# Performance work log

Hardware: AMD Instinct MI355X
Metric: run time of the kernel (lower is better)

## Reference

```python
import jax, jax.numpy as jnp
import numpy as np

B, N, IN, E, H, F = 64, 256, 128, 256, 8, 1024


def setup_inputs() -> dict:
    key = jax.random.key(0)
    ks = jax.random.split(key, 16)
    x = jax.random.normal(ks[0], (B, N, IN), jnp.float32)
    adj = (jax.random.uniform(ks[1], (B, N, N)) < 0.1).astype(jnp.float32)
    adj = jnp.maximum(adj, adj.transpose(0, 2, 1))  # symmetric 0/1 adjacency
    mask = jax.random.randint(ks[2], (B, N), 0, 2).astype(jnp.float32)
    dist = jax.random.normal(ks[3], (B, N, N), jnp.float32)

    def lin(k, i, o):
        return (jax.random.normal(k, (i, o), jnp.float32) / np.sqrt(i)).astype(jnp.float32)

    return dict(
        x=x, adj=adj, mask=mask, dist=dist,
        W1=lin(ks[4], IN, E), b1=jnp.zeros((E,), jnp.float32),
        W2=lin(ks[5], E, E), b2=jnp.zeros((E,), jnp.float32),
        W3=lin(ks[6], E, E), b3=jnp.zeros((E,), jnp.float32),
        ln1_g=jnp.ones((E,), jnp.float32), ln1_b=jnp.zeros((E,), jnp.float32),
        Wq=lin(ks[7], E, H * E), Wk=lin(ks[8], E, H * E), Wv=lin(ks[9], E, H * E),
        Wo=lin(ks[10], H * E, E), bo=jnp.zeros((E,), jnp.float32),
        ln2_g=jnp.ones((E,), jnp.float32), ln2_b=jnp.zeros((E,), jnp.float32),
        Wf1=lin(ks[11], E, F), bf1=jnp.zeros((F,), jnp.float32),
        Wf2=lin(ks[12], F, E), bf2=jnp.zeros((E,), jnp.float32),
    )


def _layernorm(x, g, b):
    m = x.mean(-1, keepdims=True)
    v = ((x - m) ** 2).mean(-1, keepdims=True)
    return (x - m) * jax.lax.rsqrt(v + 1e-5) * g + b


def reference(x, adj, mask, dist, W1, b1, W2, b2, W3, b3, ln1_g, ln1_b,
              Wq, Wk, Wv, Wo, bo, ln2_g, ln2_b, Wf1, bf1, Wf2, bf2):
    # --- DenseGCNConv normalization (add self-loops, sym-normalize) ---
    eye = jnp.eye(N, dtype=adj.dtype)
    A = adj * (1.0 - eye) + eye                      # fill_diag(adj, 1)
    dis = jax.lax.rsqrt(jnp.clip(A.sum(-1), 1.0, None))
    An = dis[:, :, None] * A * dis[:, None, :]       # D^-1/2 A D^-1/2, [B,N,N]
    m3 = mask[:, :, None]

    def gcn(h, W, b):
        return (jnp.einsum('bij,bjf->bif', An, h @ W) + b) * m3

    g1 = jax.nn.relu(gcn(x, W1, b1))
    g2 = jax.nn.relu(gcn(g1, W2, b2))
    g3 = jax.nn.relu(gcn(g2, W3, b3))
    gcn_res = g1 + g2 + g3

    # --- masked MHA with distance bias (head dim = E per head) ---
    h = _layernorm(gcn_res, ln1_g, ln1_b)
    mh = mask[:, None, :, None]                      # [B,1,N,1]
    q = (h @ Wq).reshape(B, N, H, E).transpose(0, 2, 1, 3) * mh
    k = (h @ Wk).reshape(B, N, H, E).transpose(0, 2, 1, 3) * mh
    v = (h @ Wv).reshape(B, N, H, E).transpose(0, 2, 1, 3) * mh
    a = jnp.einsum('bhne,bhme->bhnm', q * (E ** -0.5), k) + dist[:, None]
    am = (mask[:, :, None] * mask[:, None, :])[:, None]  # [B,1,N,N]
    a = jnp.where(am == 0, -1e9, a)
    a = jax.nn.softmax(a, axis=-1)
    a = jnp.where(am == 0, 0.0, a)
    y = jnp.einsum('bhnm,bhme->bhne', a, v).transpose(0, 2, 1, 3).reshape(B, N, H * E)
    y = (y @ Wo + bo) * m3
    att = gcn_res + y

    # --- FFN block ---
    f = _layernorm(att, ln2_g, ln2_b)
    f = (jax.nn.gelu(f @ Wf1 + bf1, approximate=False) @ Wf2 + bf2) * m3
    att = att + f
    return gcn_res + att
```

## Files before the change

### kernel.cpp

```cpp
#include <hip/hip_runtime.h>
#include <hip/hip_bf16.h>
#include <cmath>

#define BB 64
#define NNODES 256
#define INF_ 128
#define EE 256
#define HH 8
#define FFN 1024
#define BNROWS 16384

typedef __attribute__((ext_vector_type(8))) short short8;
typedef __attribute__((ext_vector_type(4))) float floatx4;
typedef __attribute__((ext_vector_type(4))) unsigned short ushort4v;

__device__ __forceinline__ float b2f(unsigned short u) {
  union { unsigned u32; float f; } w; w.u32 = ((unsigned)u) << 16; return w.f;
}
__device__ __forceinline__ unsigned short f2b(float f) {
  union { float f; unsigned u32; } w; w.f = f;
  unsigned r = w.u32 + 0x7FFFu + ((w.u32 >> 16) & 1u);
  return (unsigned short)(r >> 16);
}
__device__ __forceinline__ float gelu_f(float x) {
  const float z = 0.7978845608028654f * (x + 0.044715f * x * x * x);
  const float e = __expf(2.0f * z);
  const float th = (e - 1.0f) / (e + 1.0f);
  return 0.5f * x * (1.0f + th);
}

typedef const __attribute__((address_space(1))) void GV;
typedef __attribute__((address_space(3))) void LV;

__device__ __forceinline__ void gl_lds16(const unsigned short* g,
                                         unsigned short* l, int lane) {
#if __has_builtin(__builtin_amdgcn_global_load_lds)
  __builtin_amdgcn_global_load_lds((GV*)g, (LV*)l, 16, 0, 0);
#else
  *(short8*)(l + lane * 8) = *(const short8*)g;
#endif
}

#define VMW2() asm volatile("s_waitcnt vmcnt(2)" ::: "memory")
#define VMW0() asm volatile("s_waitcnt vmcnt(0)" ::: "memory")
#define LGW0() asm volatile("s_waitcnt lgkmcnt(0)" ::: "memory")
#define MBAR() do { asm volatile("" ::: "memory"); \
                    __builtin_amdgcn_s_barrier(); \
                    asm volatile("" ::: "memory"); } while (0)

struct PackArgs {
  const float* src[12];
  unsigned short* dst[12];
  int R[12], C[12];
  int start[13];
};

__launch_bounds__(256)
__global__ void pack_kernel(PackArgs a)
{
  __shared__ float tile[32][33];
  const int bid = blockIdx.x;
  int j = 0;
  while (bid >= a.start[j + 1]) j++;
  const int lb = bid - a.start[j];
  const float* src = a.src[j];
  unsigned short* dst = a.dst[j];
  const int R = a.R[j], C = a.C[j];

  if (C == 0) {
    const int i = (lb * 256 + threadIdx.x) * 4;
    if (i >= R) return;
    floatx4 v = *(const floatx4*)(src + i);
    ushort4v o;
    #pragma unroll
    for (int k = 0; k < 4; k++) o[k] = f2b(v[k]);
    *(ushort4v*)(dst + i) = o;
    return;
  }
  const int tpr = C >> 5;
  const int c0 = (lb % tpr) * 32, r0 = (lb / tpr) * 32;
  const int tx = threadIdx.x & 31, ty = threadIdx.x >> 5;
  #pragma unroll
  for (int i = ty; i < 32; i += 8)
    tile[i][tx] = src[(long long)(r0 + i) * C + c0 + tx];
  __syncthreads();
  #pragma unroll
  for (int i = ty; i < 32; i += 8)
    dst[(long long)(c0 + i) * R + r0 + tx] = f2b(tile[tx][i]);
}

__global__ void deg_kernel(const float* __restrict__ adj,
                           float* __restrict__ dis)
{
  const int g = blockIdx.x * 4 + (threadIdx.x >> 6);
  const int lane = threadIdx.x & 63;
  const int i = g & 255;
  floatx4 v = *(const floatx4*)(adj + (long long)g * 256 + lane * 4);
  float s = 0.f;
  #pragma unroll
  for (int jj = 0; jj < 4; jj++) {
    const int j = lane * 4 + jj;
    s += (j == i) ? 1.0f : v[jj];
  }
  #pragma unroll
  for (int off = 32; off > 0; off >>= 1) s += __shfl_xor(s, off);
  if (lane == 0) dis[g] = 1.0f / sqrtf(fmaxf(s, 1.0f));
}

__global__ void an_kernel(const float* __restrict__ adj,
                          const float* __restrict__ dis,
                          unsigned short* __restrict__ An)
{
  const long long base = ((long long)blockIdx.x * 256 + threadIdx.x) * 4;
  const int rowg = (int)(base >> 8);
  const int i = rowg & 255;
  const int brow = rowg & ~255;
  const int j0 = (int)(base & 255);
  const float di = dis[rowg];
  floatx4 v = *(const floatx4*)(adj + base);
  ushort4v o;
  #pragma unroll
  for (int jj = 0; jj < 4; jj++) {
    const int j = j0 + jj;
    const float a = (j == i) ? 1.0f : v[jj];
    o[jj] = f2b(di * dis[brow + j] * a);
  }
  *(ushort4v*)(An + base) = o;
}

__launch_bounds__(512, 4)
__global__ void gemm_kernel(const unsigned short* __restrict__ A, int lda,
                            long long sAo, long long sAi,
                            const unsigned short* __restrict__ Bm, int ldb,
                            long long sBo, long long sBi,
                            void* __restrict__ Cv, int ldc,
                            long long sCo, long long sCi,
                            int K, int zshift, int mode, int flag,
                            const float* __restrict__ aux1,
                            const float* __restrict__ mask,
                            float* __restrict__ gcn,
                            void* __restrict__ aux2)
{
  __shared__ __align__(16) unsigned short sA[16384];
  __shared__ __align__(16) unsigned short sB[16384];

  const int t = threadIdx.x;
  const int z = blockIdx.z;
  const int zi = z & ((1 << zshift) - 1);
  const int zb = z >> zshift;
  const int m0 = blockIdx.x * 128;
  const int n0 = blockIdx.y * 128;
  A  += zb * sAo + zi * sAi;
  Bm += zb * sBo + zi * sBi;
  const long long cbase = zb * sCo + zi * sCi;

  const int lane = t & 63;
  const int w = t >> 6;
  const int wm = w >> 2, wn = w & 3;
  const int lm = lane & 15, qd = lane >> 4;

  floatx4 acc[4][2] = {};

  const int sub = lane >> 4;
  const int qs  = lane & 15;
  const unsigned short* pA[4];
  const unsigned short* pB[4];
  #pragma unroll
  for (int i = 0; i < 4; i++) {
    const int d = w * 4 + i;
    const int r = d * 4 + sub;
    const int co = (qs ^ (r & 7)) * 8;
    pA[i] = A + (long long)(m0 + r) * lda + co;
    pB[i] = Bm + (long long)(n0 + r) * ldb + co;
  }

  for (int kk = 0; kk < K; kk += 128) {
    #pragma unroll
    for (int i = 0; i < 4; i++) {
      gl_lds16(pA[i] + kk, &sA[(w * 4 + i) * 512], lane);
      gl_lds16(pB[i] + kk, &sB[(w * 4 + i) * 512], lane);
    }
    __syncthreads();

    #pragma unroll
    for (int ks = 0; ks < 4; ks++) {
      short8 af[4], bg[2];
      const int q = ks * 4 + qd;
      #pragma unroll
      for (int mi = 0; mi < 4; mi++) {
        const int r = wm * 64 + mi * 16 + lm;
        af[mi] = *(const short8*)&sA[r * 128 + ((q ^ (r & 7)) * 8)];
      }
      #pragma unroll
      for (int ni = 0; ni < 2; ni++) {
        const int r = wn * 32 + ni * 16 + lm;
        bg[ni] = *(const short8*)&sB[r * 128 + ((q ^ (r & 7)) * 8)];
      }
      #pragma unroll
      for (int mi = 0; mi < 4; mi++)
        #pragma unroll
        for (int ni = 0; ni < 2; ni++)
          acc[mi][ni] = __builtin_amdgcn_mfma_f32_16x16x32_bf16(
              af[mi], bg[ni], acc[mi][ni], 0, 0, 0);
    }
    __syncthreads();
  }

  #pragma unroll
  for (int mi = 0; mi < 4; mi++) {
    const int row0 = m0 + wm * 64 + mi * 16 + qd * 4;
    #pragma unroll
    for (int ni = 0; ni < 2; ni++) {
      const int col = n0 + wn * 32 + ni * 16 + lm;
      floatx4 a = acc[mi][ni];
      if (mode == 0) {
        float* Cf = (float*)Cv;
        #pragma unroll
        for (int r = 0; r < 4; r++)
          Cf[cbase + (long long)(row0 + r) * ldc + col] = a[r];
      } else if (mode == 1) {
        unsigned short* Cb = (unsigned short*)Cv;
        #pragma unroll
        for (int r = 0; r < 4; r++)
          Cb[cbase + (long long)(row0 + r) * ldc + col] = f2b(a[r]);
      } else if (mode == 2) {
        float* Cf = (float*)Cv;
        #pragma unroll
        for (int r = 0; r < 4; r++)
          Cf[cbase + (long long)(row0 + r) * ldc + col] += a[r];
      } else if (mode == 3) {
        unsigned short* Cb = (unsigned short*)Cv;
        const float bv = aux1[col];
        #pragma unroll
        for (int r = 0; r < 4; r++)
          Cb[cbase + (long long)(row0 + r) * ldc + col] = f2b(gelu_f(a[r] + bv));
      } else if (mode == 5) {
        const int b = row0 >> 8, n = row0 & 255;
        ushort4v o;
        #pragma unroll
        for (int r = 0; r < 4; r++) o[r] = f2b(a[r]);
        *(ushort4v*)((unsigned short*)Cv + (long long)b * 65536 + col * 256 + n) = o;
      } else if (mode == 8) {
        float* Cf = (float*)Cv;
        const float* attf = (const float*)aux2;
        const float bv = aux1[col];
        #pragma unroll
        for (int r = 0; r < 4; r++) {
          const long long idx = (long long)(row0 + r) * 256 + col;
          Cf[idx] = gcn[idx] + attf[idx] + (a[r] + bv) * mask[row0 + r];
        }
      } else if (mode == 9) {
        const int token = zb * 256 + col;
        const float m = mask[token];
        ushort4v o; floatx4 g;
        #pragma unroll
        for (int r = 0; r < 4; r++) {
          const float v = fmaxf((a[r] + aux1[row0 + r]) * m, 0.f);
          o[r] = f2b(v); g[r] = v;
        }
        *(ushort4v*)((unsigned short*)Cv + (long long)token * 256 + row0) = o;
        float* gp = gcn + (long long)token * 256 + row0;
        if (flag) { floatx4 old = *(const floatx4*)gp; g += old; }
        *(floatx4*)gp = g;
      } else if (mode == 12) {
        float* Cf = (float*)Cv;
        const float bv = aux1[col];
        #pragma unroll
        for (int r = 0; r < 4; r++) {
          const long long idx = (long long)(row0 + r) * 256 + col;
          Cf[idx] = gcn[idx] + (a[r] + bv) * mask[row0 + r];
        }
      } else if (mode == 13) {
        unsigned short* Cb = (unsigned short*)Cv;
        #pragma unroll
        for (int r = 0; r < 4; r++)
          Cb[cbase + (long long)(row0 + r) * ldc + col] = f2b(a[r] * 0.0625f);
      } else {
        const int z2 = (row0 >> 8) * 8 + (col >> 8);
        const int e = col & 255, n = row0 & 255;
        ushort4v o;
        #pragma unroll
        for (int r = 0; r < 4; r++) o[r] = f2b(a[r]);
        *(ushort4v*)((unsigned short*)aux2 + (long long)z2 * 65536 + e * 256 + n) = o;
      }
    }
  }
}

__launch_bounds__(512, 4)
__global__ void attn_kernel(unsigned short* __restrict__ QP,
                            const unsigned short* __restrict__ HBF,
                            const unsigned short* __restrict__ ABH,
                            const unsigned short* __restrict__ VT,
                            const unsigned short* __restrict__ DSTB,
                            const float* __restrict__ mask)
{
  __shared__ __align__(16) unsigned short sR0[16896];
  __shared__ __align__(16) unsigned short sS[16384];
  __shared__ float redm[4][64];
  __shared__ float reds[4][64];

  const int bi = blockIdx.x;
  const int x  = bi & 7;
  const int seq = bi >> 3;
  const int b  = (seq >> 5) * 8 + x;
  const int h  = (seq >> 2) & 7;
  const int mt = seq & 3;
  const int m0 = mt * 64;
  const int z = b * 8 + h;

  const int t = threadIdx.x, lane = t & 63, w = t >> 6;
  const int lm = lane & 15, qd = lane >> 4;
  const int wm2 = w >> 2, wn4 = w & 3;

  unsigned short* Ym = QP + ((long long)(b * 256 + m0)) * 2048 + h * 256;
  const unsigned short* Hb = HBF + (long long)b * 65536;
  const unsigned short* Hq = Hb + (long long)m0 * 256;
  const unsigned short* Ah = ABH + (long long)h * 65536;
  const unsigned short* Vb = VT + (long long)z * 65536;
  const unsigned short* db = DSTB + (long long)b * 65536 + (long long)m0 * 256;
  const float* maskb = mask + b * 256;

  floatx4 S[2][4];
  #pragma unroll
  for (int mi = 0; mi < 2; mi++)
    #pragma unroll
    for (int ni = 0; ni < 4; ni++) {
      const int col = wn4 * 64 + ni * 16 + lm;
      #pragma unroll
      for (int r = 0; r < 4; r++) {
        const int row = wm2 * 32 + mi * 16 + qd * 4 + r;
        S[mi][ni][r] = b2f(db[row * 256 + col]);
      }
    }

  int eoff0, eoff1;
  {
    const int rA = lane >> 2, sl = lane & 3;
    const int r0 = (w * 2 + 0) * 16 + rA;
    const int r1 = (w * 2 + 1) * 16 + rA;
    eoff0 = r0 * 256 + ((sl ^ ((r0 >> 1) & 3)) * 8);
    eoff1 = r1 * 256 + ((sl ^ ((r1 >> 1) & 3)) * 8);
  }
  const int ld0 = (w * 2 + 0) * 512;
  const int ld1 = (w * 2 + 1) * 512;

  auto STAGE = [&](int c) {
    const unsigned short* bp =
        (c < 8 ? Ah : (c < 16 ? Hb : Vb)) + (c & 7) * 32;
    const int bb = (c & 1) * 8192;
    gl_lds16(bp + eoff0, &sS[bb + ld0], lane);
    gl_lds16(bp + eoff1, &sS[bb + ld1], lane);
  };

  {
    const int rin2 = lane >> 5, qs32 = lane & 31;
    #pragma unroll
    for (int i = 0; i < 4; i++) {
      const int d = w * 4 + i;
      const int r = d * 2 + rin2;
      gl_lds16(Hq + (long long)r * 256 + ((qs32 ^ (r & 7)) * 8),
               &sR0[d * 512], lane);
    }
  }
  STAGE(0); STAGE(1);
  VMW2();
  MBAR();

  floatx4 accq[2][4] = {};
  #pragma unroll
  for (int c = 0; c < 8; c++) {
    __builtin_amdgcn_s_setprio(1);
    short8 af[2], bg[4];
    #pragma unroll
    for (int mi = 0; mi < 2; mi++) {
      const int r = wm2 * 32 + mi * 16 + lm;
      const int q = c * 4 + qd;
      af[mi] = *(const short8*)&sR0[r * 256 + ((q ^ (r & 7)) * 8)];
    }
    const int bb = (c & 1) * 8192;
    #pragma unroll
    for (int ni = 0; ni < 4; ni++) {
      const int rr = wn4 * 64 + ni * 16 + lm;
      bg[ni] = *(const short8*)&sS[bb + rr * 32 + ((qd ^ ((rr >> 1) & 3)) * 8)];
    }
    #pragma unroll
    for (int mi = 0; mi < 2; mi++)
      #pragma unroll
      for (int ni = 0; ni < 4; ni++)
        accq[mi][ni] = __builtin_amdgcn_mfma_f32_16x16x32_bf16(
            af[mi], bg[ni], accq[mi][ni], 0, 0, 0);
    __builtin_amdgcn_s_setprio(0);
    MBAR();
    STAGE(c + 2);
    VMW2();
    MBAR();
  }

  #pragma unroll
  for (int mi = 0; mi < 2; mi++)
    #pragma unroll
    for (int rr = 0; rr < 4; rr++) {
      const int row = wm2 * 32 + mi * 16 + qd * 4 + rr;
      #pragma unroll
      for (int ni = 0; ni < 4; ni++) {
        const int col = wn4 * 64 + ni * 16 + lm;
        const int o = col >> 3;
        sR0[row * 256 + ((o ^ (row & 7)) * 8) + (col & 7)] = f2b(accq[mi][ni][rr]);
      }
    }
  LGW0();
  MBAR();

  #pragma unroll
  for (int c = 8; c < 16; c++) {
    __builtin_amdgcn_s_setprio(1);
    short8 af[2], bg[4];
    #pragma unroll
    for (int mi = 0; mi < 2; mi++) {
      const int r = wm2 * 32 + mi * 16 + lm;
      const int q = (c - 8) * 4 + qd;
      af[mi] = *(const short8*)&sR0[r * 256 + ((q ^ (r & 7)) * 8)];
    }
    const int bb = (c & 1) * 8192;
    #pragma unroll
    for (int ni = 0; ni < 4; ni++) {
      const int rr = wn4 * 64 + ni * 16 + lm;
      bg[ni] = *(const short8*)&sS[bb + rr * 32 + ((qd ^ ((rr >> 1) & 3)) * 8)];
    }
    #pragma unroll
    for (int mi = 0; mi < 2; mi++)
      #pragma unroll
      for (int ni = 0; ni < 4; ni++)
        S[mi][ni] = __builtin_amdgcn_mfma_f32_16x16x32_bf16(
            af[mi], bg[ni], S[mi][ni], 0, 0, 0);
    __builtin_amdgcn_s_setprio(0);
    MBAR();
    STAGE(c + 2);
    VMW2();
    MBAR();
  }

  float mkv[4];
  #pragma unroll
  for (int ni = 0; ni < 4; ni++) mkv[ni] = maskb[wn4 * 64 + ni * 16 + lm];

  float lred[2][4];
  #pragma unroll
  for (int mi = 0; mi < 2; mi++) {
    #pragma unroll
    for (int r = 0; r < 4; r++) {
      const int row = wm2 * 32 + mi * 16 + qd * 4 + r;
      const float mq = maskb[m0 + row];
      float mx = -3e38f;
      #pragma unroll
      for (int ni = 0; ni < 4; ni++) {
        const float v = (mq != 0.f && mkv[ni] != 0.f) ? S[mi][ni][r] : -1e9f;
        S[mi][ni][r] = v;
        mx = fmaxf(mx, v);
      }
      lred[mi][r] = mx;
    }
  }
  #pragma unroll
  for (int off = 1; off < 16; off <<= 1)
    #pragma unroll
    for (int mi = 0; mi < 2; mi++)
      #pragma unroll
      for (int r = 0; r < 4; r++)
        lred[mi][r] = fmaxf(lred[mi][r], __shfl_xor(lred[mi][r], off));
  if (lm == 0)
    #pragma unroll
    for (int mi = 0; mi < 2; mi++)
      #pragma unroll
      for (int r = 0; r < 4; r++)
        redm[wn4][wm2 * 32 + mi * 16 + qd * 4 + r] = lred[mi][r];
  LGW0();
  MBAR();

  #pragma unroll
  for (int mi = 0; mi < 2; mi++) {
    #pragma unroll
    for (int r = 0; r < 4; r++) {
      const int row = wm2 * 32 + mi * 16 + qd * 4 + r;
      const float gmax = fmaxf(fmaxf(redm[0][row], redm[1][row]),
                               fmaxf(redm[2][row], redm[3][row]));
      float ss = 0.f;
      #pragma unroll
      for (int ni = 0; ni < 4; ni++) {
        const float e = __expf(S[mi][ni][r] - gmax);
        S[mi][ni][r] = e;
        ss += e;
      }
      lred[mi][r] = ss;
    }
  }
  #pragma unroll
  for (int off = 1; off < 16; off <<= 1)
    #pragma unroll
    for (int mi = 0; mi < 2; mi++)
      #pragma unroll
      for (int r = 0; r < 4; r++)
        lred[mi][r] += __shfl_xor(lred[mi][r], off);
  if (lm == 0)
    #pragma unroll
    for (int mi = 0; mi < 2; mi++)
      #pragma unroll
      for (int r = 0; r < 4; r++)
        reds[wn4][wm2 * 32 + mi * 16 + qd * 4 + r] = lred[mi][r];
  LGW0();
  MBAR();

  #pragma unroll
  for (int mi = 0; mi < 2; mi++)
    #pragma unroll
    for (int r = 0; r < 4; r++) {
      const int row = wm2 * 32 + mi * 16 + qd * 4 + r;
      const float inv = 1.0f / (reds[0][row] + reds[1][row] +
                                reds[2][row] + reds[3][row]);
      #pragma unroll
      for (int ni = 0; ni < 4; ni++) {
        const int kl = ni * 16 + lm;
        const int slot = (kl >> 3) ^ (row & 7);
        sR0[wn4 * 4096 + row * 64 + slot * 8 + (kl & 7)] =
            f2b(S[mi][ni][r] * inv);
      }
    }
  LGW0();
  MBAR();

  floatx4 Y[2][4] = {};
  #pragma unroll
  for (int c = 16; c < 24; c++) {
    __builtin_amdgcn_s_setprio(1);
    const int pp = (c - 16) >> 1;
    const int op = ((c - 16) & 1) * 4 + qd;
    short8 af[2], bg[4];
    #pragma unroll
    for (int mi = 0; mi < 2; mi++) {
      const int r = wm2 * 32 + mi * 16 + lm;
      af[mi] = *(const short8*)&sR0[pp * 4096 + r * 64 + ((op ^ (r & 7)) * 8)];
    }
    const int bb = (c & 1) * 8192;
    #pragma unroll
    for (int ni = 0; ni < 4; ni++) {
      const int rr = wn4 * 64 + ni * 16 + lm;
      bg[ni] = *(const short8*)&sS[bb + rr * 32 + ((qd ^ ((rr >> 1) & 3)) * 8)];
    }
    #pragma unroll
    for (int mi = 0; mi < 2; mi++)
      #pragma unroll
      for (int ni = 0; ni < 4; ni++)
        Y[mi][ni] = __builtin_amdgcn_mfma_f32_16x16x32_bf16(
            af[mi], bg[ni], Y[mi][ni], 0, 0, 0);
    __builtin_amdgcn_s_setprio(0);
    MBAR();
    if (c < 22) {
      STAGE(c + 2);
      VMW2();
      MBAR();
    } else if (c == 22) {
      VMW0();
      MBAR();
    }
  }

  #pragma unroll
  for (int mi = 0; mi < 2; mi++)
    #pragma unroll
    for (int ni = 0; ni < 4; ni++) {
      const int col = wn4 * 64 + ni * 16 + lm;
      #pragma unroll
      for (int r = 0; r < 4; r++) {
        const int rl = wm2 * 32 + mi * 16 + qd * 4 + r;
        sR0[rl * 264 + col] = f2b(Y[mi][ni][r]);
      }
    }
  LGW0();
  MBAR();
  #pragma unroll
  for (int it = 0; it < 4; it++) {
    const int idx = it * 512 + t;
    const int row = idx >> 5, u = idx & 31;
    short8 v = *(const short8*)&sR0[row * 264 + u * 8];
    *(short8*)(Ym + (long long)row * 2048 + u * 8) = v;
  }
}

__global__ void ln_kernel(const float* __restrict__ X,
                          const float* __restrict__ gam,
                          const float* __restrict__ bet,
                          unsigned short* __restrict__ out)
{
  const int g = blockIdx.x * 4 + (threadIdx.x >> 6);
  const int lane = threadIdx.x & 63;
  floatx4 v = *(const floatx4*)(X + (long long)g * 256 + lane * 4);
  float s = v[0] + v[1] + v[2] + v[3];
  float sq = v[0]*v[0] + v[1]*v[1] + v[2]*v[2] + v[3]*v[3];
  #pragma unroll
  for (int off = 32; off > 0; off >>= 1) {
    s  += __shfl_xor(s, off);
    sq += __shfl_xor(sq, off);
  }
  const float mean = s * (1.0f / 256.0f);
  const float var = sq * (1.0f / 256.0f) - mean * mean;
  const float rs = 1.0f / sqrtf(var + 1e-5f);
  ushort4v o;
  #pragma unroll
  for (int jj = 0; jj < 4; jj++) {
    const int c = lane * 4 + jj;
    o[jj] = f2b((v[jj] - mean) * rs * gam[c] + bet[c]);
  }
  *(ushort4v*)(out + (long long)g * 256 + lane * 4) = o;
}

static inline void launch_gemm(hipStream_t st, int M, int N, int batch,
    const void* A, int lda, long long sAo, long long sAi,
    const void* B, int ldb, long long sBo, long long sBi,
    void* C, int ldc, long long sCo, long long sCi,
    int K, int zshift, int mode, int flag,
    const float* aux1, const float* mask, float* gcn, void* aux2)
{
  dim3 grid(M / 128, N / 128, batch), blk(512);
  gemm_kernel<<<grid, blk, 0, st>>>(
      (const unsigned short*)A, lda, sAo, sAi,
      (const unsigned short*)B, ldb, sBo, sBi,
      C, ldc, sCo, sCi, K, zshift, mode, flag, aux1, mask, gcn, aux2);
}

extern "C" void kernel_launch(void* const* d_in, const int* in_sizes, int n_in,
                              void* d_out, int out_size, void* d_ws, size_t ws_size,
                              hipStream_t stream)
{
  (void)in_sizes; (void)n_in; (void)out_size;
  const float* x    = (const float*)d_in[0];
  const float* adj  = (const float*)d_in[1];
  const float* mask = (const float*)d_in[2];
  const float* dist = (const float*)d_in[3];
  const float* W1   = (const float*)d_in[4];
  const float* b1   = (const float*)d_in[5];
  const float* W2   = (const float*)d_in[6];
  const float* b2   = (const float*)d_in[7];
  const float* W3   = (const float*)d_in[8];
  const float* b3   = (const float*)d_in[9];
  const float* ln1g = (const float*)d_in[10];
  const float* ln1b = (const float*)d_in[11];
  const float* Wq   = (const float*)d_in[12];
  const float* Wk   = (const float*)d_in[13];
  const float* Wv   = (const float*)d_in[14];
  const float* Wo   = (const float*)d_in[15];
  const float* bo   = (const float*)d_in[16];
  const float* ln2g = (const float*)d_in[17];
  const float* ln2b = (const float*)d_in[18];
  const float* Wf1  = (const float*)d_in[19];
  const float* bf1  = (const float*)d_in[20];
  const float* Wf2  = (const float*)d_in[21];
  const float* bf2  = (const float*)d_in[22];

  char* w = (char*)d_ws;
  auto alloc = [&](size_t sz) { void* p = (void*)w; w += sz; return p; };
  unsigned short* W1T   = (unsigned short*)alloc(65536);
  unsigned short* W2T   = (unsigned short*)alloc(131072);
  unsigned short* W3T   = (unsigned short*)alloc(131072);
  unsigned short* ABH   = (unsigned short*)alloc(1048576);
  unsigned short* WVT   = (unsigned short*)alloc(1048576);
  unsigned short* WOT   = (unsigned short*)alloc(1048576);
  unsigned short* WF1T  = (unsigned short*)alloc(524288);
  unsigned short* WF2T  = (unsigned short*)alloc(524288);
  unsigned short* WQb   = (unsigned short*)alloc(1048576);
  unsigned short* WKb   = (unsigned short*)alloc(1048576);
  unsigned short* XBF   = (unsigned short*)alloc(4194304);
  unsigned short* DSTB  = (unsigned short*)alloc(8388608);
  float*          GCN   = (float*)         alloc(16777216);
  float*          U     = (float*)         alloc(16777216);
  unsigned short* HBF   = (unsigned short*)alloc(8388608);
  float*          DIS   = (float*)         alloc(65536);
  char* scratch = (char*)alloc(134217728);
  if ((size_t)(w - (char*)d_ws) > ws_size) return;
  unsigned short* AN  = (unsigned short*)scratch;
  unsigned short* TT  = (unsigned short*)(scratch + 8388608);
  unsigned short* GBF = (unsigned short*)(scratch + 16777216);
  unsigned short* QPB = (unsigned short*)scratch;
  unsigned short* VT  = (unsigned short*)(scratch + 67108864);
  unsigned short* FFB = (unsigned short*)scratch;

  PackArgs pa;
  const float* srcs[11] = {W1, W2, W3, Wv, Wo, Wf1, Wf2, x, Wq, Wk, dist};
  unsigned short* dsts[11] = {W1T, W2T, W3T, WVT, WOT, WF1T, WF2T, XBF, WQb, WKb, DSTB};
  const int Rs[11] = {128, 256, 256, 256, 2048, 256, 1024,
                      BNROWS * INF_, EE * HH * EE, EE * HH * EE, BB * 65536};
  const int Cs[11] = {256, 256, 256, 2048, 256, 1024, 256, 0, 0, 0, 0};
  const int sts[12] = {0, 32, 96, 160, 672, 1184, 1440, 1696, 3744, 4256, 4768, 8864};
  for (int j = 0; j < 11; j++) {
    pa.src[j] = srcs[j]; pa.dst[j] = dsts[j]; pa.R[j] = Rs[j]; pa.C[j] = Cs[j];
  }
  for (int j = 0; j < 12; j++) pa.start[j] = sts[j];
  pack_kernel<<<8864, 256, 0, stream>>>(pa);

  deg_kernel<<<4096, 256, 0, stream>>>(adj, DIS);
  an_kernel<<<4096, 256, 0, stream>>>(adj, DIS, AN);

  launch_gemm(stream, 256, 256, 8, WKb, 2048, 256, 0, WQb, 2048, 256, 0,
              ABH, 256, 65536, 0, 256, 0, 13, 0, nullptr, nullptr, nullptr, nullptr);

  launch_gemm(stream, BNROWS, EE, 1, XBF, 128, 0,0, W1T, 128, 0,0,
              TT, 256, 0,0, 128, 0, 5, 0, nullptr, nullptr, nullptr, nullptr);
  launch_gemm(stream, 256, 256, BB, TT, 256, 65536,0, AN, 256, 65536,0,
              GBF, 256, 0,0, 256, 0, 9, 0, b1, mask, GCN, nullptr);
  launch_gemm(stream, BNROWS, EE, 1, GBF, 256, 0,0, W2T, 256, 0,0,
              TT, 256, 0,0, 256, 0, 5, 0, nullptr, nullptr, nullptr, nullptr);
  launch_gemm(stream, 256, 256, BB, TT, 256, 65536,0, AN, 256, 65536,0,
              GBF, 256, 0,0, 256, 0, 9, 1, b2, mask, GCN, nullptr);
  launch_gemm(stream, BNROWS, EE, 1, GBF, 256, 0,0, W3T, 256, 0,0,
              TT, 256, 0,0, 256, 0, 5, 0, nullptr, nullptr, nullptr, nullptr);
  launch_gemm(stream, 256, 256, BB, TT, 256, 65536,0, AN, 256, 65536,0,
              GBF, 256, 0,0, 256, 0, 9, 1, b3, mask, GCN, nullptr);

  ln_kernel<<<4096, 256, 0, stream>>>(GCN, ln1g, ln1b, HBF);

  launch_gemm(stream, BNROWS, 2048, 1, HBF, 256, 0,0, WVT, 256, 0,0,
              QPB, 2048, 0,0, 256, 0, 16, 0, nullptr, nullptr, nullptr, VT);
  attn_kernel<<<2048, 512, 0, stream>>>(QPB, HBF, ABH, VT, DSTB, mask);
  launch_gemm(stream, BNROWS, EE, 1, QPB, 2048, 0,0, WOT, 2048, 0,0,
              U, 256, 0,0, 2048, 0, 12, 0, bo, mask, GCN, nullptr);

  ln_kernel<<<4096, 256, 0, stream>>>(U, ln2g, ln2b, HBF);
  launch_gemm(stream, BNROWS, FFN, 1, HBF, 256, 0,0, WF1T, 256, 0,0,
              FFB, 1024, 0,0, 256, 0, 3, 0, bf1, nullptr, nullptr, nullptr);
  launch_gemm(stream, BNROWS, EE, 1, FFB, 1024, 0,0, WF2T, 1024, 0,0,
              d_out, 256, 0,0, 1024, 0, 8, 0, bf2, mask, GCN, U);
}
```

Before: 453.0 us.

## Triple-buffer attention LDS staging to drop one barrier per k-step

```diff
diff --git a/kernel.cpp b/kernel.cpp
--- a/kernel.cpp
+++ b/kernel.cpp
@@ -295,10 +295,8 @@
                             const unsigned short* __restrict__ DSTB,
                             const float* __restrict__ mask)
 {
-  __shared__ __align__(16) unsigned short sR0[16896];
-  __shared__ __align__(16) unsigned short sS[16384];
-  __shared__ float redm[4][64];
-  __shared__ float reds[4][64];
+  __shared__ __align__(16) unsigned short sR0[16384];
+  __shared__ __align__(16) unsigned short sS[24576];
 
   const int bi = blockIdx.x;
   const int x  = bi & 7;
@@ -321,6 +319,8 @@
   const unsigned short* db = DSTB + (long long)b * 65536 + (long long)m0 * 256;
   const float* maskb = mask + b * 256;
 
+  float* redf = (float*)sS;
+
   floatx4 S[2][4];
   #pragma unroll
   for (int mi = 0; mi < 2; mi++)
@@ -348,7 +348,7 @@
   auto STAGE = [&](int c) {
     const unsigned short* bp =
         (c < 8 ? Ah : (c < 16 ? Hb : Vb)) + (c & 7) * 32;
-    const int bb = (c & 1) * 8192;
+    const int bb = (c % 3) * 8192;
     gl_lds16(bp + eoff0, &sS[bb + ld0], lane);
     gl_lds16(bp + eoff1, &sS[bb + ld1], lane);
   };
@@ -364,12 +364,12 @@
     }
   }
   STAGE(0); STAGE(1);
-  VMW2();
-  MBAR();
 
   floatx4 accq[2][4] = {};
   #pragma unroll
   for (int c = 0; c < 8; c++) {
+    VMW2();
+    MBAR();
     __builtin_amdgcn_s_setprio(1);
     short8 af[2], bg[4];
     #pragma unroll
@@ -378,7 +378,7 @@
       const int q = c * 4 + qd;
       af[mi] = *(const short8*)&sR0[r * 256 + ((q ^ (r & 7)) * 8)];
     }
-    const int bb = (c & 1) * 8192;
+    const int bb = (c % 3) * 8192;
     #pragma unroll
     for (int ni = 0; ni < 4; ni++) {
       const int rr = wn4 * 64 + ni * 16 + lm;
@@ -391,12 +391,10 @@
         accq[mi][ni] = __builtin_amdgcn_mfma_f32_16x16x32_bf16(
             af[mi], bg[ni], accq[mi][ni], 0, 0, 0);
     __builtin_amdgcn_s_setprio(0);
-    MBAR();
     STAGE(c + 2);
-    VMW2();
-    MBAR();
-  }
-
+  }
+
+  MBAR();
   #pragma unroll
   for (int mi = 0; mi < 2; mi++)
     #pragma unroll
@@ -410,10 +408,11 @@
       }
     }
   LGW0();
-  MBAR();
 
   #pragma unroll
   for (int c = 8; c < 16; c++) {
+    VMW2();
+    MBAR();
     __builtin_amdgcn_s_setprio(1);
     short8 af[2], bg[4];
     #pragma unroll
@@ -422,7 +421,7 @@
       const int q = (c - 8) * 4 + qd;
       af[mi] = *(const short8*)&sR0[r * 256 + ((q ^ (r & 7)) * 8)];
     }
-    const int bb = (c & 1) * 8192;
+    const int bb = (c % 3) * 8192;
     #pragma unroll
     for (int ni = 0; ni < 4; ni++) {
       const int rr = wn4 * 64 + ni * 16 + lm;
@@ -435,12 +434,10 @@
         S[mi][ni] = __builtin_amdgcn_mfma_f32_16x16x32_bf16(
             af[mi], bg[ni], S[mi][ni], 0, 0, 0);
     __builtin_amdgcn_s_setprio(0);
-    MBAR();
     STAGE(c + 2);
-    VMW2();
-    MBAR();
-  }
-
+  }
+
+  MBAR();
   float mkv[4];
   #pragma unroll
   for (int ni = 0; ni < 4; ni++) mkv[ni] = maskb[wn4 * 64 + ni * 16 + lm];
@@ -474,7 +471,7 @@
     for (int mi = 0; mi < 2; mi++)
       #pragma unroll
       for (int r = 0; r < 4; r++)
-        redm[wn4][wm2 * 32 + mi * 16 + qd * 4 + r] = lred[mi][r];
+        redf[wn4 * 64 + wm2 * 32 + mi * 16 + qd * 4 + r] = lred[mi][r];
   LGW0();
   MBAR();
 
@@ -483,8 +480,8 @@
     #pragma unroll
     for (int r = 0; r < 4; r++) {
       const int row = wm2 * 32 + mi * 16 + qd * 4 + r;
-      const float gmax = fmaxf(fmaxf(redm[0][row], redm[1][row]),
-                               fmaxf(redm[2][row], redm[3][row]));
+      const float gmax = fmaxf(fmaxf(redf[row], redf[64 + row]),
+                               fmaxf(redf[128 + row], redf[192 + row]));
       float ss = 0.f;
       #pragma unroll
       for (int ni = 0; ni < 4; ni++) {
@@ -507,7 +504,7 @@
     for (int mi = 0; mi < 2; mi++)
       #pragma unroll
       for (int r = 0; r < 4; r++)
-        reds[wn4][wm2 * 32 + mi * 16 + qd * 4 + r] = lred[mi][r];
+        redf[256 + wn4 * 64 + wm2 * 32 + mi * 16 + qd * 4 + r] = lred[mi][r];
   LGW0();
   MBAR();
 
@@ -516,8 +513,8 @@
     #pragma unroll
     for (int r = 0; r < 4; r++) {
       const int row = wm2 * 32 + mi * 16 + qd * 4 + r;
-      const float inv = 1.0f / (reds[0][row] + reds[1][row] +
-                                reds[2][row] + reds[3][row]);
+      const float inv = 1.0f / (redf[256 + row] + redf[320 + row] +
+                                redf[384 + row] + redf[448 + row]);
       #pragma unroll
       for (int ni = 0; ni < 4; ni++) {
         const int kl = ni * 16 + lm;
@@ -527,11 +524,12 @@
       }
     }
   LGW0();
-  MBAR();
 
   floatx4 Y[2][4] = {};
   #pragma unroll
   for (int c = 16; c < 24; c++) {
+    if (c < 23) { VMW2(); } else { VMW0(); }
+    MBAR();
     __builtin_amdgcn_s_setprio(1);
     const int pp = (c - 16) >> 1;
     const int op = ((c - 16) & 1) * 4 + qd;
@@ -541,7 +539,7 @@
       const int r = wm2 * 32 + mi * 16 + lm;
       af[mi] = *(const short8*)&sR0[pp * 4096 + r * 64 + ((op ^ (r & 7)) * 8)];
     }
-    const int bb = (c & 1) * 8192;
+    const int bb = (c % 3) * 8192;
     #pragma unroll
     for (int ni = 0; ni < 4; ni++) {
       const int rr = wn4 * 64 + ni * 16 + lm;
@@ -554,17 +552,10 @@
         Y[mi][ni] = __builtin_amdgcn_mfma_f32_16x16x32_bf16(
             af[mi], bg[ni], Y[mi][ni], 0, 0, 0);
     __builtin_amdgcn_s_setprio(0);
-    MBAR();
-    if (c < 22) {
-      STAGE(c + 2);
-      VMW2();
-      MBAR();
-    } else if (c == 22) {
-      VMW0();
-      MBAR();
-    }
-  }
-
+    if (c < 22) STAGE(c + 2);
+  }
+
+  MBAR();
   #pragma unroll
   for (int mi = 0; mi < 2; mi++)
     #pragma unroll
@@ -572,8 +563,9 @@
       const int col = wn4 * 64 + ni * 16 + lm;
       #pragma unroll
       for (int r = 0; r < 4; r++) {
-        const int rl = wm2 * 32 + mi * 16 + qd * 4 + r;
-        sR0[rl * 264 + col] = f2b(Y[mi][ni][r]);
+        const int row = wm2 * 32 + mi * 16 + qd * 4 + r;
+        sR0[row * 256 + (((col >> 3) ^ (row & 7)) * 8) + (col & 7)] =
+            f2b(Y[mi][ni][r]);
       }
     }
   LGW0();
@@ -582,7 +574,7 @@
   for (int it = 0; it < 4; it++) {
     const int idx = it * 512 + t;
     const int row = idx >> 5, u = idx & 31;
-    short8 v = *(const short8*)&sR0[row * 264 + u * 8];
+    short8 v = *(const short8*)&sR0[row * 256 + ((u ^ (row & 7)) * 8)];
     *(short8*)(Ym + (long long)row * 2048 + u * 8) = v;
   }
 }
```

Result: no change. 449.6 us (-0.7%).

## Single-buffer attention B-operand staging to raise occupancy

Applied to the files above, without the earlier changes.

```diff
diff --git a/kernel.cpp b/kernel.cpp
--- a/kernel.cpp
+++ b/kernel.cpp
@@ -41,7 +41,6 @@
 #endif
 }
 
-#define VMW2() asm volatile("s_waitcnt vmcnt(2)" ::: "memory")
 #define VMW0() asm volatile("s_waitcnt vmcnt(0)" ::: "memory")
 #define LGW0() asm volatile("s_waitcnt lgkmcnt(0)" ::: "memory")
 #define MBAR() do { asm volatile("" ::: "memory"); \
@@ -287,7 +286,7 @@
   }
 }
 
-__launch_bounds__(512, 4)
+__launch_bounds__(512, 6)
 __global__ void attn_kernel(unsigned short* __restrict__ QP,
                             const unsigned short* __restrict__ HBF,
                             const unsigned short* __restrict__ ABH,
@@ -296,7 +295,7 @@
                             const float* __restrict__ mask)
 {
   __shared__ __align__(16) unsigned short sR0[16896];
-  __shared__ __align__(16) unsigned short sS[16384];
+  __shared__ __align__(16) unsigned short sS[8192];
   __shared__ float redm[4][64];
   __shared__ float reds[4][64];
 
@@ -348,9 +347,8 @@
   auto STAGE = [&](int c) {
     const unsigned short* bp =
         (c < 8 ? Ah : (c < 16 ? Hb : Vb)) + (c & 7) * 32;
-    const int bb = (c & 1) * 8192;
-    gl_lds16(bp + eoff0, &sS[bb + ld0], lane);
-    gl_lds16(bp + eoff1, &sS[bb + ld1], lane);
+    gl_lds16(bp + eoff0, &sS[ld0], lane);
+    gl_lds16(bp + eoff1, &sS[ld1], lane);
   };
 
   {
@@ -363,13 +361,13 @@
                &sR0[d * 512], lane);
     }
   }
-  STAGE(0); STAGE(1);
-  VMW2();
-  MBAR();
 
   floatx4 accq[2][4] = {};
   #pragma unroll
   for (int c = 0; c < 8; c++) {
+    STAGE(c);
+    VMW0();
+    MBAR();
     __builtin_amdgcn_s_setprio(1);
     short8 af[2], bg[4];
     #pragma unroll
@@ -378,11 +376,10 @@
       const int q = c * 4 + qd;
       af[mi] = *(const short8*)&sR0[r * 256 + ((q ^ (r & 7)) * 8)];
     }
-    const int bb = (c & 1) * 8192;
     #pragma unroll
     for (int ni = 0; ni < 4; ni++) {
       const int rr = wn4 * 64 + ni * 16 + lm;
-      bg[ni] = *(const short8*)&sS[bb + rr * 32 + ((qd ^ ((rr >> 1) & 3)) * 8)];
+      bg[ni] = *(const short8*)&sS[rr * 32 + ((qd ^ ((rr >> 1) & 3)) * 8)];
     }
     #pragma unroll
     for (int mi = 0; mi < 2; mi++)
@@ -392,9 +389,6 @@
             af[mi], bg[ni], accq[mi][ni], 0, 0, 0);
     __builtin_amdgcn_s_setprio(0);
     MBAR();
-    STAGE(c + 2);
-    VMW2();
-    MBAR();
   }
 
   #pragma unroll
@@ -414,6 +408,9 @@
 
   #pragma unroll
   for (int c = 8; c < 16; c++) {
+    STAGE(c);
+    VMW0();
+    MBAR();
     __builtin_amdgcn_s_setprio(1);
     short8 af[2], bg[4];
     #pragma unroll
@@ -422,11 +419,10 @@
       const int q = (c - 8) * 4 + qd;
       af[mi] = *(const short8*)&sR0[r * 256 + ((q ^ (r & 7)) * 8)];
     }
-    const int bb = (c & 1) * 8192;
     #pragma unroll
     for (int ni = 0; ni < 4; ni++) {
       const int rr = wn4 * 64 + ni * 16 + lm;
-      bg[ni] = *(const short8*)&sS[bb + rr * 32 + ((qd ^ ((rr >> 1) & 3)) * 8)];
+      bg[ni] = *(const short8*)&sS[rr * 32 + ((qd ^ ((rr >> 1) & 3)) * 8)];
     }
     #pragma unroll
     for (int mi = 0; mi < 2; mi++)
@@ -436,9 +432,6 @@
             af[mi], bg[ni], S[mi][ni], 0, 0, 0);
     __builtin_amdgcn_s_setprio(0);
     MBAR();
-    STAGE(c + 2);
-    VMW2();
-    MBAR();
   }
 
   float mkv[4];
@@ -532,6 +525,9 @@
   floatx4 Y[2][4] = {};
   #pragma unroll
   for (int c = 16; c < 24; c++) {
+    STAGE(c);
+    VMW0();
+    MBAR();
     __builtin_amdgcn_s_setprio(1);
     const int pp = (c - 16) >> 1;
     const int op = ((c - 16) & 1) * 4 + qd;
@@ -541,11 +537,10 @@
       const int r = wm2 * 32 + mi * 16 + lm;
       af[mi] = *(const short8*)&sR0[pp * 4096 + r * 64 + ((op ^ (r & 7)) * 8)];
     }
-    const int bb = (c & 1) * 8192;
     #pragma unroll
     for (int ni = 0; ni < 4; ni++) {
       const int rr = wn4 * 64 + ni * 16 + lm;
-      bg[ni] = *(const short8*)&sS[bb + rr * 32 + ((qd ^ ((rr >> 1) & 3)) * 8)];
+      bg[ni] = *(const short8*)&sS[rr * 32 + ((qd ^ ((rr >> 1) & 3)) * 8)];
     }
     #pragma unroll
     for (int mi = 0; mi < 2; mi++)
@@ -555,14 +550,6 @@
             af[mi], bg[ni], Y[mi][ni], 0, 0, 0);
     __builtin_amdgcn_s_setprio(0);
     MBAR();
-    if (c < 22) {
-      STAGE(c + 2);
-      VMW2();
-      MBAR();
-    } else if (c == 22) {
-      VMW0();
-      MBAR();
-    }
   }
 
   #pragma unroll
```

Result: slower. 533.6 us (+17.8%).
